# Performance work log

Measured on AMD Instinct MI355X. Metric: run time of the kernel, lower is better.

The kernel has to match this reference:

```python
import jax, jax.numpy as jnp
import numpy as np

B, C, N, K, COUT, W32 = 4, 64, 4096, 16, 64, 32
EPS = 1e-5  # BatchNorm eps


def conv1x1(x, w, b):
    # x: (B, Cin, K, N), w: (Cout, Cin), b: (Cout,)
    return jnp.einsum('oi,bikn->bokn', w, x) + b[None, :, None, None]


def batchnorm(x, gamma, beta):
    # training-mode BN over (B, K, N) per channel
    m = x.mean(axis=(0, 2, 3), keepdims=True)
    v = x.var(axis=(0, 2, 3), keepdims=True)
    return gamma[None, :, None, None] * (x - m) * jax.lax.rsqrt(v + EPS) + beta[None, :, None, None]


def setup_inputs() -> dict:
    key = jax.random.key(0)
    ks = jax.random.split(key, 14)
    s = 0.1
    return {
        'inputs': jax.random.normal(ks[0], (B, C, N), jnp.float32),
        'inputs_pos': jax.random.normal(ks[1], (B, 3, N), jnp.float32),
        'inverse_density': jax.random.uniform(ks[2], (B, 1, N), jnp.float32),
        # WeightNet: Conv2d(3, 32, 1) + BN(32)
        'wn_w': jax.random.normal(ks[3], (W32, 3), jnp.float32) * s,
        'wn_b': jnp.zeros((W32,), jnp.float32),
        'wn_g': jnp.ones((W32,), jnp.float32),
        'wn_be': jnp.zeros((W32,), jnp.float32),
        # DensityNet: Conv2d(1,16,1)+BN(16), Conv2d(16,1,1)
        'dn_w1': jax.random.normal(ks[4], (16, 1), jnp.float32) * s,
        'dn_b1': jnp.zeros((16,), jnp.float32),
        'dn_g1': jnp.ones((16,), jnp.float32),
        'dn_be1': jnp.zeros((16,), jnp.float32),
        'dn_w2': jax.random.normal(ks[5], (1, 16), jnp.float32) * s,
        'dn_b2': jnp.zeros((1,), jnp.float32),
        # Linear(C*32, COUT)
        'lin_w': jax.random.normal(ks[6], (COUT, C * W32), jnp.float32) * (1.0 / np.sqrt(C * W32)),
        'lin_b': jnp.zeros((COUT,), jnp.float32),
    }


def reference(inputs, inputs_pos, inverse_density,
              wn_w, wn_b, wn_g, wn_be,
              dn_w1, dn_b1, dn_g1, dn_be1, dn_w2, dn_b2,
              lin_w, lin_b):
    b, c, n = inputs.shape
    # pairwise squared distances (B, N, N); stride=1 so no FPS sampling
    sq = jnp.sum(inputs_pos ** 2, axis=1)  # (B, N)
    dist = sq[:, :, None] + sq[:, None, :] - 2.0 * jnp.einsum('bdi,bdj->bij', inputs_pos, inputs_pos)
    _, nn_idx = jax.lax.top_k(-dist, K)  # (B, N, K) nearest neighbors (incl. self)

    def gather(x, idx):  # x: (Cx, N), idx: (N, K) -> (Cx, K, N)
        return jnp.transpose(x[:, idx], (0, 2, 1))

    nn_pos = jax.vmap(gather)(inputs_pos, nn_idx)        # (B, 3, K, N)
    nn_inputs = jax.vmap(gather)(inputs, nn_idx)         # (B, C, K, N)
    lnn_pos = nn_pos - inputs_pos[:, :, None, :]         # translated neighbor positions
    nn_inv_d = jax.vmap(gather)(inverse_density, nn_idx)  # (B, 1, K, N)

    density_scale = nn_inv_d / nn_inv_d.max(axis=2, keepdims=True)
    h = jax.nn.relu(batchnorm(conv1x1(density_scale, dn_w1, dn_b1), dn_g1, dn_be1))
    density_scale = jax.nn.sigmoid(conv1x1(h, dn_w2, dn_b2))  # (B, 1, K, N)

    scaled = nn_inputs * density_scale                    # (B, C, K, N)
    weights = jax.nn.relu(batchnorm(conv1x1(lnn_pos, wn_w, wn_b), wn_g, wn_be))  # (B, 32, K, N)

    # per-point matmul: (B,N,C,K) @ (B,N,K,32) -> (B,N,C,32)
    feat = jnp.einsum('bckn,bwkn->bncw', scaled, weights).reshape(b, n, c * W32)
    out = feat @ lin_w.T + lin_b                          # (B, N, COUT)
    return jnp.transpose(out, (0, 2, 1))                  # (B, COUT, N)
```

## Files before the change

kernel.cpp:

```cpp
#include <hip/hip_runtime.h>
#include <math.h>

#define NB 4
#define NC 64
#define NPTS 4096
#define NROWS (NB*NPTS)

typedef __attribute__((ext_vector_type(4))) float f32x4;
typedef __bf16 bf16x8 __attribute__((ext_vector_type(8)));

__device__ __forceinline__ ushort f2bf(float f) {
  unsigned u = __float_as_uint(f);
  u = (u + 0x7FFFu + ((u >> 16) & 1u)) >> 16;
  return (ushort)u;
}
__device__ __forceinline__ unsigned pk2(float lo, float hi) {
  return (unsigned)f2bf(lo) | ((unsigned)f2bf(hi) << 16);
}

__device__ __forceinline__ void insert16(double dist, int j, double (&dd)[16], int (&ii)[16]) {
  double cd = dist; int ci = j;
#pragma unroll
  for (int s = 0; s < 16; ++s) {
    double od = dd[s]; int oi = ii[s];
    bool c = cd < od;
    dd[s] = c ? cd : od;
    ii[s] = c ? ci : oi;
    cd = c ? od : cd;
    ci = c ? oi : ci;
  }
}

__device__ __forceinline__ void bub16u(unsigned key, unsigned (&t)[16]) {
#pragma unroll
  for (int q2 = 0; q2 < 16; ++q2) {
    unsigned lo = min(key, t[q2]);
    key = max(key, t[q2]);
    t[q2] = lo;
  }
}

#define DPPD(RES, V, CTRL) { \
  long long bits_ = __double_as_longlong(V); \
  int lo_ = (int)bits_, hi_ = (int)(bits_ >> 32); \
  int lo2_ = __builtin_amdgcn_update_dpp(0, lo_, CTRL, 0xF, 0xF, true); \
  int hi2_ = __builtin_amdgcn_update_dpp(0, hi_, CTRL, 0xF, 0xF, true); \
  RES = __longlong_as_double(((long long)(unsigned)lo2_) | ((long long)hi2_ << 32)); }

__device__ __forceinline__ double wave_reduce(double v) {
  double t2;
  DPPD(t2, v, 0x121) v += t2;
  DPPD(t2, v, 0x122) v += t2;
  DPPD(t2, v, 0x124) v += t2;
  DPPD(t2, v, 0x128) v += t2;
  v += __shfl_xor(v, 16, 64);
  v += __shfl_xor(v, 32, 64);
  return v;
}

__global__ __launch_bounds__(256) void prep_all(const float* __restrict__ pos,
                                                float4* __restrict__ pos4,
                                                const float* __restrict__ in,
                                                ushort* __restrict__ inT,
                                                const float* __restrict__ lin_w,
                                                ushort* __restrict__ LTf) {
  __shared__ float tile[64][68];
  int t = threadIdx.x;
  int bid = blockIdx.x;
  if (bid < 64) {
    int g = bid * 256 + t;
    int b = g >> 12, n = g & (NPTS - 1);
    const float* pb = pos + b * 3 * NPTS;
    pos4[g] = make_float4(pb[n], pb[NPTS + n], pb[2 * NPTS + n], 0.f);
  } else if (bid < 320) {
    int blk = bid - 64;
    int b = blk >> 6;
    int n0 = (blk & 63) << 6;
    {
      int c = t >> 2, q = t & 3;
      const float* src = in + ((size_t)(b * 64 + c)) * NPTS + n0 + q * 16;
      float4 v0 = ((const float4*)src)[0];
      float4 v1 = ((const float4*)src)[1];
      float4 v2 = ((const float4*)src)[2];
      float4 v3 = ((const float4*)src)[3];
      *(float4*)&tile[c][q * 16 + 0] = v0;
      *(float4*)&tile[c][q * 16 + 4] = v1;
      *(float4*)&tile[c][q * 16 + 8] = v2;
      *(float4*)&tile[c][q * 16 + 12] = v3;
    }
    __syncthreads();
    {
      int nl = t >> 2, cq = t & 3;
      unsigned pk[8];
#pragma unroll
      for (int i = 0; i < 8; ++i) {
        float lo = tile[cq * 16 + 2 * i][nl];
        float hi = tile[cq * 16 + 2 * i + 1][nl];
        pk[i] = pk2(lo, hi);
      }
      uint4* dst = (uint4*)(inT + ((size_t)(b * NPTS + n0 + nl)) * 64 + cq * 16);
      dst[0] = make_uint4(pk[0], pk[1], pk[2], pk[3]);
      dst[1] = make_uint4(pk[4], pk[5], pk[6], pk[7]);
    }
  } else {
    int g = (bid - 320) * 256 + t;
    int l = g & 63, ot = (g >> 6) & 3, s = g >> 8;
    int o = ot * 16 + (l & 15);
    const float* src = lin_w + (size_t)o * 2048 + s * 32 + (l >> 4) * 8;
    float4 u0 = ((const float4*)src)[0];
    float4 u1 = ((const float4*)src)[1];
    ((uint4*)LTf)[g] = make_uint4(pk2(u0.x, u0.y), pk2(u0.z, u0.w),
                                  pk2(u1.x, u1.y), pk2(u1.z, u1.w));
  }
}

__global__ __launch_bounds__(256) void knn_sub(const float4* __restrict__ pos4,
                                               uint4* __restrict__ partials) {
  __shared__ float4 cand[128];
  int t = threadIdx.x;
  int row0 = blockIdx.x * 256;
  int b = row0 >> 12;
  int y = blockIdx.y;
  int j0 = (y >> 1) * 1024 + (y & 1) * 128;
  const float4* pb = pos4 + b * NPTS;
  if (t < 128) cand[t] = pb[j0 + t];
  __syncthreads();
  float4 q = pb[(row0 + t) & (NPTS - 1)];
  unsigned dd[16];
#pragma unroll
  for (int s = 0; s < 16; ++s) dd[s] = 0xFFFFFFFFu;
#pragma unroll 4
  for (int jj = 0; jj < 128; ++jj) {
    float4 c = cand[jj];
    float dx = q.x - c.x, dy = q.y - c.y, dz = q.z - c.z;
    float d = fmaf(dx, dx, fmaf(dy, dy, dz * dz));
    unsigned key = (__float_as_uint(d) & 0xFFFFF000u) | (unsigned)(j0 + jj);
#pragma unroll
    for (int s = 0; s < 16; ++s) {
      unsigned lo = min(key, dd[s]);
      key = max(key, dd[s]);
      dd[s] = lo;
    }
  }
  uint4* po = partials + ((size_t)y * NROWS + row0 + t) * 4;
  po[0] = make_uint4(dd[0], dd[1], dd[2], dd[3]);
  po[1] = make_uint4(dd[4], dd[5], dd[6], dd[7]);
  po[2] = make_uint4(dd[8], dd[9], dd[10], dd[11]);
  po[3] = make_uint4(dd[12], dd[13], dd[14], dd[15]);
}

__global__ __launch_bounds__(64) void knn_thresh(const uint4* __restrict__ partials,
                                                 unsigned* __restrict__ T0g) {
  __shared__ unsigned sl[64 * 132];
  int tid = threadIdx.x;
  int row0 = blockIdx.x * 64;
  uint4* sl4 = (uint4*)sl;
  size_t base = (size_t)row0 * 4 + tid;
#define TW(IT, V) { int g2 = ((IT) & 3) * 64 + tid; \
                    sl4[(g2 >> 2) * 33 + ((IT) >> 2) * 4 + (g2 & 3)] = (V); }
#define TB(B) { int IT0 = (B) * 8; \
  uint4 w0 = partials[(size_t)((IT0+0)>>2)*(NROWS*4) + ((IT0+0)&3)*64 + base]; \
  uint4 w1 = partials[(size_t)((IT0+1)>>2)*(NROWS*4) + ((IT0+1)&3)*64 + base]; \
  uint4 w2 = partials[(size_t)((IT0+2)>>2)*(NROWS*4) + ((IT0+2)&3)*64 + base]; \
  uint4 w3 = partials[(size_t)((IT0+3)>>2)*(NROWS*4) + ((IT0+3)&3)*64 + base]; \
  uint4 w4 = partials[(size_t)((IT0+4)>>2)*(NROWS*4) + ((IT0+4)&3)*64 + base]; \
  uint4 w5 = partials[(size_t)((IT0+5)>>2)*(NROWS*4) + ((IT0+5)&3)*64 + base]; \
  uint4 w6 = partials[(size_t)((IT0+6)>>2)*(NROWS*4) + ((IT0+6)&3)*64 + base]; \
  uint4 w7 = partials[(size_t)((IT0+7)>>2)*(NROWS*4) + ((IT0+7)&3)*64 + base]; \
  TW(IT0+0,w0) TW(IT0+1,w1) TW(IT0+2,w2) TW(IT0+3,w3) \
  TW(IT0+4,w4) TW(IT0+5,w5) TW(IT0+6,w6) TW(IT0+7,w7) }
  TB(0) TB(1) TB(2) TB(3)
#undef TB
#undef TW
  __syncthreads();
  unsigned top[16];
#pragma unroll
  for (int s = 0; s < 16; ++s) top[s] = 0xFFFFFFFFu;
  const unsigned* my = sl + tid * 132;
  for (int y = 0; y < 8; ++y) {
#pragma unroll 4
    for (int s = 0; s < 16; ++s) {
      unsigned key = my[y * 16 + s];
      if (key >= top[15]) break;
#pragma unroll
      for (int q2 = 0; q2 < 16; ++q2) {
        unsigned lo = min(key, top[q2]);
        key = max(key, top[q2]);
        top[q2] = lo;
      }
    }
  }
  T0g[row0 + tid] = top[15] & 0xFFFFF000u;
}

__global__ __launch_bounds__(256) void knn_filter(const float4* __restrict__ pos4,
                                                  const unsigned* __restrict__ T0g,
                                                  uint4* __restrict__ surv) {
  __shared__ float4 cand[256];
  __shared__ unsigned lq[256 * 28];
  int t = threadIdx.x;
  int row0 = blockIdx.x * 256;
  int b = row0 >> 12;
  int y = blockIdx.y;
  int j0 = y * 256;
  const float4* pb = pos4 + b * NPTS;
  cand[t] = pb[j0 + t];
  __syncthreads();
  int r = row0 + t;
  float4 q = pb[r & (NPTS - 1)];
  unsigned T = T0g[r];
  unsigned cnt = 0;
  unsigned* myq = lq + t * 28;
#pragma unroll 4
  for (int jj = 0; jj < 256; ++jj) {
    float4 c = cand[jj];
    float dx = q.x - c.x, dy = q.y - c.y, dz = q.z - c.z;
    float d = fmaf(dx, dx, fmaf(dy, dy, dz * dz));
    unsigned m = __float_as_uint(d) & 0xFFFFF000u;
    if (m <= T) {
      if (cnt < 28u) myq[cnt] = m | (unsigned)(j0 + jj);
      ++cnt;
    }
  }
  cnt = cnt < 28u ? cnt : 28u;
  unsigned t16[16];
#pragma unroll
  for (int s = 0; s < 16; ++s) t16[s] = 0xFFFFFFFFu;
  const uint4* qsrc = (const uint4*)myq;
  uint4 q0 = qsrc[0], q1 = qsrc[1], q2 = qsrc[2], q3 = qsrc[3],
        q4 = qsrc[4], q5 = qsrc[5], q6 = qsrc[6];
#define SIN(K, I) { if ((I) < cnt) bub16u((K), t16); }
  SIN(q0.x,0u) SIN(q0.y,1u) SIN(q0.z,2u) SIN(q0.w,3u)
  SIN(q1.x,4u) SIN(q1.y,5u) SIN(q1.z,6u) SIN(q1.w,7u)
  SIN(q2.x,8u) SIN(q2.y,9u) SIN(q2.z,10u) SIN(q2.w,11u)
  SIN(q3.x,12u) SIN(q3.y,13u) SIN(q3.z,14u) SIN(q3.w,15u)
  SIN(q4.x,16u) SIN(q4.y,17u) SIN(q4.z,18u) SIN(q4.w,19u)
  SIN(q5.x,20u) SIN(q5.y,21u) SIN(q5.z,22u) SIN(q5.w,23u)
  SIN(q6.x,24u) SIN(q6.y,25u) SIN(q6.z,26u) SIN(q6.w,27u)
#undef SIN
  uint4* dst = surv + ((size_t)r * 16 + y) * 4;
  dst[0] = make_uint4(t16[0], t16[1], t16[2], t16[3]);
  dst[1] = make_uint4(t16[4], t16[5], t16[6], t16[7]);
  dst[2] = make_uint4(t16[8], t16[9], t16[10], t16[11]);
  dst[3] = make_uint4(t16[12], t16[13], t16[14], t16[15]);
}

__global__ __launch_bounds__(256) void knn_final(const float4* __restrict__ pos4,
                                                 const float* __restrict__ invd,
                                                 const uint4* __restrict__ surv,
                                                 int* __restrict__ nn_idx,
                                                 float* __restrict__ dsbuf,
                                                 double* __restrict__ stp) {
  int t = threadIdx.x;
  int ln = t & 15;
  int r = blockIdx.x * 16 + (t >> 4);
  int b = r >> 12, n = r & (NPTS - 1);

  const uint4* sp = surv + ((size_t)r * 16 + ln) * 4;
  uint4 u0 = sp[0], u1 = sp[1], u2 = sp[2], u3 = sp[3];
  unsigned h0=u0.x,h1=u0.y,h2=u0.z,h3=u0.w,h4=u1.x,h5=u1.y,h6=u1.z,h7=u1.w,
           h8=u2.x,h9=u2.y,h10=u2.z,h11=u2.w,h12=u3.x,h13=u3.y,h14=u3.z,h15=u3.w;
  unsigned t0,t1,t2,t3,t4,t5,t6,t7,t8,t9,t10,t11,t12,t13,t14,t15,t16;
#define UMIN_DPP(M, CTRL) \
  M = min(M, (unsigned)__builtin_amdgcn_update_dpp(0, (int)(M), CTRL, 0xF, 0xF, true));
#define RND(TT) { unsigned m = h0; \
  UMIN_DPP(m, 0x121) UMIN_DPP(m, 0x122) UMIN_DPP(m, 0x124) UMIN_DPP(m, 0x128) \
  TT = m; bool pop = (h0 == m); \
  h0 = pop ? h1 : h0;  h1 = pop ? h2 : h1;  h2 = pop ? h3 : h2; \
  h3 = pop ? h4 : h3;  h4 = pop ? h5 : h4;  h5 = pop ? h6 : h5; \
  h6 = pop ? h7 : h6;  h7 = pop ? h8 : h7;  h8 = pop ? h9 : h8; \
  h9 = pop ? h10 : h9; h10 = pop ? h11 : h10; h11 = pop ? h12 : h11; \
  h12 = pop ? h13 : h12; h13 = pop ? h14 : h13; h14 = pop ? h15 : h14; \
  h15 = pop ? 0xFFFFFFFFu : h15; }
  RND(t0) RND(t1) RND(t2) RND(t3) RND(t4) RND(t5) RND(t6) RND(t7)
  RND(t8) RND(t9) RND(t10) RND(t11) RND(t12) RND(t13) RND(t14) RND(t15)
  RND(t16)

  const float4* pb = pos4 + b * NPTS;
  float4 qp = pb[n];
  double xi = qp.x, yi = qp.y, zi = qp.z;

  int jm;
  bool tie = ((t15 & 0xFFFFF000u) == (t16 & 0xFFFFF000u));
  if (!tie) {
    unsigned tm = t0;
    tm = (ln == 1) ? t1 : tm;   tm = (ln == 2) ? t2 : tm;
    tm = (ln == 3) ? t3 : tm;   tm = (ln == 4) ? t4 : tm;
    tm = (ln == 5) ? t5 : tm;   tm = (ln == 6) ? t6 : tm;
    tm = (ln == 7) ? t7 : tm;   tm = (ln == 8) ? t8 : tm;
    tm = (ln == 9) ? t9 : tm;   tm = (ln == 10) ? t10 : tm;
    tm = (ln == 11) ? t11 : tm; tm = (ln == 12) ? t12 : tm;
    tm = (ln == 13) ? t13 : tm; tm = (ln == 14) ? t14 : tm;
    tm = (ln == 15) ? t15 : tm;
    jm = (int)(tm & 0xFFFu);
  } else {
    unsigned t17, t18, t19, t20, t21, t22, t23;
    RND(t17) RND(t18) RND(t19) RND(t20) RND(t21) RND(t22) RND(t23)
    double dd[16]; int ii[16];
#pragma unroll
    for (int s = 0; s < 16; ++s) { dd[s] = 1e300; ii[s] = 0; }
#define RRK(TT) if (TT != 0xFFFFFFFFu) { int j = (int)(TT & 0xFFFu); \
  float4 cj = pb[j]; \
  double dx = xi - (double)cj.x, dy = yi - (double)cj.y, dz = zi - (double)cj.z; \
  double dist = dx * dx + dy * dy + dz * dz; \
  if (dist < dd[15]) insert16(dist, j, dd, ii); }
    RRK(t0) RRK(t1) RRK(t2) RRK(t3) RRK(t4) RRK(t5) RRK(t6) RRK(t7)
    RRK(t8) RRK(t9) RRK(t10) RRK(t11) RRK(t12) RRK(t13) RRK(t14) RRK(t15)
    RRK(t16) RRK(t17) RRK(t18) RRK(t19) RRK(t20) RRK(t21) RRK(t22) RRK(t23)
#undef RRK
    int jj2 = ii[0];
#pragma unroll
    for (int s = 1; s < 16; ++s) jj2 = (ln == s) ? ii[s] : jj2;
    jm = jj2;
  }
#undef RND
#undef UMIN_DPP

  nn_idx[(size_t)r * 16 + ln] = jm;
  const float* ivb = invd + b * NPTS;
  float v = ivb[jm];
  float vmax = v;
#define FMAX_DPP(X, CTRL) { \
    float y_ = __int_as_float(__builtin_amdgcn_update_dpp(0, __float_as_int(X), CTRL, 0xF, 0xF, true)); \
    X = fmaxf(X, y_); }
  FMAX_DPP(vmax, 0x121) FMAX_DPP(vmax, 0x122)
  FMAX_DPP(vmax, 0x124) FMAX_DPP(vmax, 0x128)
#undef FMAX_DPP
  float x = v / vmax;
  dsbuf[(size_t)r * 16 + ln] = x;

  double sx = x, sxx = (double)x * (double)x;
  float4 pj = pb[jm];
  double lx = (double)pj.x - xi, lyv = (double)pj.y - yi, lzv = (double)pj.z - zi;
  double l1x = lx, l1y = lyv, l1z = lzv;
  double lxx = lx * lx, lyy = lyv * lyv, lzz = lzv * lzv;
  double lxy = lx * lyv, lxz = lx * lzv, lyz = lyv * lzv;
  sx  = wave_reduce(sx);  sxx = wave_reduce(sxx);
  l1x = wave_reduce(l1x); l1y = wave_reduce(l1y); l1z = wave_reduce(l1z);
  lxx = wave_reduce(lxx); lyy = wave_reduce(lyy); lzz = wave_reduce(lzz);
  lxy = wave_reduce(lxy); lxz = wave_reduce(lxz); lyz = wave_reduce(lyz);
  if ((t & 63) == 0) {
    double* o = stp + ((size_t)blockIdx.x * 4 + (t >> 6)) * 16;
    o[0] = sx;  o[1] = sxx;
    o[2] = l1x; o[3] = l1y; o[4] = l1z;
    o[5] = lxx; o[6] = lyy; o[7] = lzz;
    o[8] = lxy; o[9] = lxz; o[10] = lyz;
  }
}

__global__ __launch_bounds__(256) void finalize_params(const double* __restrict__ stp,
                                const float* __restrict__ wn_w,
                                const float* __restrict__ wn_g,
                                const float* __restrict__ wn_be,
                                const float* __restrict__ dn_w1,
                                const float* __restrict__ dn_g1,
                                const float* __restrict__ dn_be1,
                                float* __restrict__ prm) {
  __shared__ double part[16][16];
  __shared__ double red[11];
  const double M = (double)NROWS * 16.0;
  int t = threadIdx.x;
  {
    int c = t & 15, ch = t >> 4;
    double s = 0.0;
#pragma unroll 8
    for (int w = 0; w < 256; ++w) s += stp[(size_t)(ch * 256 + w) * 16 + c];
    part[ch][c] = s;
  }
  __syncthreads();
  if (t < 11) {
    double s = 0.0;
#pragma unroll
    for (int ch = 0; ch < 16; ++ch) s += part[ch][t];
    red[t] = s;
  }
  __syncthreads();
  if (t < 32) {
    double m0 = red[2] / M, m1 = red[3] / M, m2 = red[4] / M;
    double cxx = red[5] / M - m0 * m0, cyy = red[6] / M - m1 * m1, czz = red[7] / M - m2 * m2;
    double cxy = red[8] / M - m0 * m1, cxz = red[9] / M - m0 * m2, cyz = red[10] / M - m1 * m2;
    double w0 = wn_w[t * 3], w1 = wn_w[t * 3 + 1], w2 = wn_w[t * 3 + 2];
    double var = w0 * w0 * cxx + w1 * w1 * cyy + w2 * w2 * czz
               + 2.0 * (w0 * w1 * cxy + w0 * w2 * cxz + w1 * w2 * cyz);
    double alpha = (double)wn_g[t] / sqrt(var + 1e-5);
    double a0 = alpha * w0, a1 = alpha * w1, a2 = alpha * w2;
    prm[t * 3] = (float)a0; prm[t * 3 + 1] = (float)a1; prm[t * 3 + 2] = (float)a2;
    prm[96 + t] = (float)((double)wn_be[t] - (a0 * m0 + a1 * m1 + a2 * m2));
  } else if (t < 48) {
    int ch = t - 32;
    double mx = red[0] / M;
    double vx = red[1] / M - mx * mx;
    double w = dn_w1[ch];
    double alpha = (double)dn_g1[ch] * w / sqrt(w * w * vx + 1e-5);
    prm[128 + ch] = (float)alpha;
    prm[144 + ch] = (float)((double)dn_be1[ch] - alpha * mx);
  }
}

#define XSTR 2320
#define WTOFF 37120
#define WTSTR 1040

__global__ __launch_bounds__(256, 3) void fused(const ushort* __restrict__ inT,
                                                const float4* __restrict__ pos4,
                                                const int* __restrict__ nn_idx,
                                                const float* __restrict__ dsbuf,
                                                const float* __restrict__ prm_g,
                                                const float* __restrict__ dn_w2,
                                                const float* __restrict__ dn_b2,
                                                const ushort* __restrict__ LTf,
                                                const float* __restrict__ lin_b,
                                                float* __restrict__ out) {
  __shared__ __align__(16) char smem[53760];
  char* xraw = smem;
  char* wT = smem + WTOFF;
  int t = threadIdx.x;
  int blk = blockIdx.x;
  int b = blk >> 8;
  int n0 = (blk & 255) << 4;
  {
    int k = t >> 4, p = t & 15;
    int r = blk * 16 + p;
    int n = n0 + p;
    int j = nn_idx[(size_t)r * 16 + k];
    float4 pj = pos4[b * NPTS + j];
    float4 pn = pos4[b * NPTS + n];
    float lx = pj.x - pn.x, ly = pj.y - pn.y, lz = pj.z - pn.z;
    float xr = dsbuf[(size_t)r * 16 + k];
    float sacc = dn_b2[0];
#pragma unroll
    for (int ch = 0; ch < 16; ++ch)
      sacc = fmaf(dn_w2[ch], fmaxf(fmaf(prm_g[128 + ch], xr, prm_g[144 + ch]), 0.f), sacc);
    float ds = 1.f / (1.f + expf(-sacc));
    const uint4* srcx = (const uint4*)(inT + ((size_t)(b * NPTS + j)) * 64);
    uint4* dstx = (uint4*)(xraw + p * XSTR + k * 144);
#pragma unroll
    for (int i = 0; i < 8; ++i) dstx[i] = srcx[i];
    char* wr = wT + p * WTSTR + k * 2;
#pragma unroll
    for (int w = 0; w < 32; ++w) {
      float v = fmaf(prm_g[w * 3], lx,
                fmaf(prm_g[w * 3 + 1], ly,
                fmaf(prm_g[w * 3 + 2], lz, prm_g[96 + w])));
      *(ushort*)(wr + w * 32) = f2bf(fmaxf(v, 0.f) * ds);
    }
  }
  __syncthreads();
  int wv = t >> 6;
  int l = t & 63;
  int lr = l & 15;
  int q = l >> 4;
  int kq8 = (q & 1) * 1152;
  int swz = (lr & 7) << 4;
  const f32x4 zf = (f32x4)0.f;
  uint4 zu = make_uint4(0u, 0u, 0u, 0u);

#define DECLD(IT) unsigned d##IT##_0,d##IT##_1,d##IT##_2,d##IT##_3,d##IT##_4, \
  d##IT##_5,d##IT##_6,d##IT##_7,d##IT##_8,d##IT##_9,d##IT##_10,d##IT##_11, \
  d##IT##_12,d##IT##_13,d##IT##_14,d##IT##_15;
  DECLD(0) DECLD(1) DECLD(2) DECLD(3)
#undef DECLD

#define LOADB(BU, NI, XP) { \
    const char* xb = (XP) + ((NI) * 16 + lr) * 2; \
    unsigned e0 = *(const ushort*)(xb); \
    unsigned e1 = *(const ushort*)(xb + 144); \
    unsigned e2 = *(const ushort*)(xb + 288); \
    unsigned e3 = *(const ushort*)(xb + 432); \
    unsigned e4 = *(const ushort*)(xb + 576); \
    unsigned e5 = *(const ushort*)(xb + 720); \
    unsigned e6 = *(const ushort*)(xb + 864); \
    unsigned e7 = *(const ushort*)(xb + 1008); \
    BU = make_uint4(e0 | (e1 << 16), e2 | (e3 << 16), \
                    e4 | (e5 << 16), e6 | (e7 << 16)); }

#define MM(AF, BF, RA, RB) { \
    f32x4 D = __builtin_amdgcn_mfma_f32_16x16x32_bf16(AF, BF, zf, 0, 0, 0); \
    RA = pk2(D.x, D.y); RB = pk2(D.z, D.w); }

#define DO_POINT(IT) { \
    int p = wv * 4 + (IT); \
    const char* wtp = wT + p * WTSTR; \
    const char* xp = xraw + p * XSTR + kq8; \
    uint4 a0u = zu, a1u = zu; \
    if (q < 2) { \
      a0u = *(const uint4*)(wtp + lr * 32 + q * 16); \
      a1u = *(const uint4*)(wtp + (16 + lr) * 32 + q * 16); \
    } \
    bf16x8 A0 = *reinterpret_cast<bf16x8*>(&a0u); \
    bf16x8 A1 = *reinterpret_cast<bf16x8*>(&a1u); \
    uint4 b0u, b1u, b2u, b3u; \
    LOADB(b0u, 0, xp) LOADB(b1u, 1, xp) LOADB(b2u, 2, xp) LOADB(b3u, 3, xp) \
    bf16x8 B0 = *reinterpret_cast<bf16x8*>(&b0u); \
    bf16x8 B1 = *reinterpret_cast<bf16x8*>(&b1u); \
    bf16x8 B2 = *reinterpret_cast<bf16x8*>(&b2u); \
    bf16x8 B3 = *reinterpret_cast<bf16x8*>(&b3u); \
    MM(A0, B0, d##IT##_0, d##IT##_1)   MM(A0, B1, d##IT##_2, d##IT##_3) \
    MM(A0, B2, d##IT##_4, d##IT##_5)   MM(A0, B3, d##IT##_6, d##IT##_7) \
    MM(A1, B0, d##IT##_8, d##IT##_9)   MM(A1, B1, d##IT##_10, d##IT##_11) \
    MM(A1, B2, d##IT##_12, d##IT##_13) MM(A1, B3, d##IT##_14, d##IT##_15) }

  DO_POINT(0) DO_POINT(1) DO_POINT(2) DO_POINT(3)
#undef DO_POINT
#undef MM
#undef LOADB
  __syncthreads();
  int hq = q >> 1;
  int m0 = (q & 1) * 2;
  const uint4* Lq = (const uint4*)LTf;
  f32x4 cacc = (f32x4)0.f;
#define STT(IT, MI, NIL, RA, RB) { \
    int p = wv * 4 + (IT); \
    int h = (MI) * 2 + hq; \
    int base = (((NIL) * 16 + lr)) * 1024 + (p + 16 * h) * 16 + m0 * 4; \
    *(unsigned*)(smem + (base ^ swz)) = RA; \
    *(unsigned*)(smem + ((base + 4) ^ swz)) = RB; }
#define STPA(IT) \
    STT(IT,0,0,d##IT##_0,d##IT##_1)   STT(IT,0,1,d##IT##_2,d##IT##_3) \
    STT(IT,1,0,d##IT##_8,d##IT##_9)   STT(IT,1,1,d##IT##_10,d##IT##_11)
  STPA(0) STPA(1) STPA(2) STPA(3)
#undef STPA
  __syncthreads();
#pragma unroll 4
  for (int s = 0; s < 32; ++s) {
    uint4 ua = *(const uint4*)(smem + (((s * 64 + l) * 16) ^ ((s & 7) << 4)));
    uint4 ub = Lq[(s * 4 + wv) * 64 + l];
    bf16x8 A = *reinterpret_cast<bf16x8*>(&ua);
    bf16x8 B = *reinterpret_cast<bf16x8*>(&ub);
    cacc = __builtin_amdgcn_mfma_f32_16x16x32_bf16(A, B, cacc, 0, 0, 0);
  }
  __syncthreads();
#define STPB(IT) \
    STT(IT,0,0,d##IT##_4,d##IT##_5)   STT(IT,0,1,d##IT##_6,d##IT##_7) \
    STT(IT,1,0,d##IT##_12,d##IT##_13) STT(IT,1,1,d##IT##_14,d##IT##_15)
  STPB(0) STPB(1) STPB(2) STPB(3)
#undef STPB
#undef STT
  __syncthreads();
#pragma unroll 4
  for (int sl2 = 0; sl2 < 32; ++sl2) {
    int s = sl2 + 32;
    uint4 ua = *(const uint4*)(smem + (((sl2 * 64 + l) * 16) ^ ((sl2 & 7) << 4)));
    uint4 ub = Lq[(s * 4 + wv) * 64 + l];
    bf16x8 A = *reinterpret_cast<bf16x8*>(&ua);
    bf16x8 B = *reinterpret_cast<bf16x8*>(&ub);
    cacc = __builtin_amdgcn_mfma_f32_16x16x32_bf16(A, B, cacc, 0, 0, 0);
  }
  {
    int o = wv * 16 + lr;
    float bias = lin_b[o];
    cacc.x += bias; cacc.y += bias; cacc.z += bias; cacc.w += bias;
    *(f32x4*)(out + ((size_t)(b * 64 + o)) * NPTS + n0 + q * 4) = cacc;
  }
}

extern "C" void kernel_launch(void* const* d_in, const int* in_sizes, int n_in,
                              void* d_out, int out_size, void* d_ws, size_t ws_size,
                              hipStream_t stream) {
  (void)in_sizes; (void)n_in; (void)out_size; (void)ws_size;
  const float* inputs = (const float*)d_in[0];
  const float* pos    = (const float*)d_in[1];
  const float* invd   = (const float*)d_in[2];
  const float* wn_w   = (const float*)d_in[3];
  const float* wn_g   = (const float*)d_in[5];
  const float* wn_be  = (const float*)d_in[6];
  const float* dn_w1  = (const float*)d_in[7];
  const float* dn_g1  = (const float*)d_in[9];
  const float* dn_be1 = (const float*)d_in[10];
  const float* dn_w2  = (const float*)d_in[11];
  const float* dn_b2  = (const float*)d_in[12];
  const float* lin_w  = (const float*)d_in[13];
  const float* lin_b  = (const float*)d_in[14];
  float* outp = (float*)d_out;

  char* ws = (char*)d_ws;
  float*    prm      = (float*)(ws + 1024);
  float4*   pos4     = (float4*)(ws + 4096);
  int*      nnidx    = (int*)(ws + (size_t)(1u << 19));
  float*    dsbuf    = (float*)(ws + (size_t)(3u << 19));
  ushort*   inT      = (ushort*)(ws + (size_t)(5u << 19));
  ushort*   LTf      = (ushort*)(ws + (size_t)(9u << 19));
  unsigned* T0g      = (unsigned*)(ws + (size_t)(19u << 18));
  double*   stp      = (double*)(ws + (size_t)(5u << 20));
  uint4*    partials = (uint4*)(ws + (size_t)(11u << 19));
  uint4*    surv     = (uint4*)(ws + (size_t)(11u << 19));

  prep_all<<<384, 256, 0, stream>>>(pos, pos4, inputs, inT, lin_w, LTf);
  knn_sub<<<dim3(64, 8), 256, 0, stream>>>(pos4, partials);
  knn_thresh<<<256, 64, 0, stream>>>(partials, T0g);
  knn_filter<<<dim3(64, 16), 256, 0, stream>>>(pos4, T0g, surv);
  knn_final<<<1024, 256, 0, stream>>>(pos4, invd, surv, nnidx, dsbuf, stp);
  finalize_params<<<1, 256, 0, stream>>>(stp, wn_w, wn_g, wn_be, dn_w1, dn_g1, dn_be1, prm);
  fused<<<1024, 256, 0, stream>>>(inT, pos4, nnidx, dsbuf, prm, dn_w2, dn_b2, LTf, lin_b, outp);
}
```

Measured before the change: 136.4 us.

## Fuse KNN filter and final merge into one kernel, dropping survivor buffer

Merges the threshold-filter pass and the cross-segment merge into a single kernel. Each 16-lane group now handles one query row, and each lane scans one 256-candidate segment. All 4096 batch positions are staged into LDS as padded SoA arrays, so the per-segment top-16 lists stay in registers and feed the DPP merge directly. This removes the global survivor buffer write/read and one launch. In exchange each block redundantly loads the whole batch's positions and uses about 77 KB of LDS, which limits occupancy.

```diff
diff --git a/kernel.cpp b/kernel.cpp
--- a/kernel.cpp
+++ b/kernel.cpp
@@ -193,28 +193,39 @@
   T0g[row0 + tid] = top[15] & 0xFFFFF000u;
 }
 
-__global__ __launch_bounds__(256) void knn_filter(const float4* __restrict__ pos4,
-                                                  const unsigned* __restrict__ T0g,
-                                                  uint4* __restrict__ surv) {
-  __shared__ float4 cand[256];
+__global__ __launch_bounds__(256, 2) void knn_ff(const float4* __restrict__ pos4,
+                                                 const float* __restrict__ invd,
+                                                 const unsigned* __restrict__ T0g,
+                                                 int* __restrict__ nn_idx,
+                                                 float* __restrict__ dsbuf,
+                                                 double* __restrict__ stp) {
+  __shared__ float cx[16 * 258], cy[16 * 258], cz[16 * 258];
   __shared__ unsigned lq[256 * 28];
   int t = threadIdx.x;
-  int row0 = blockIdx.x * 256;
-  int b = row0 >> 12;
-  int y = blockIdx.y;
-  int j0 = y * 256;
+  int blk = blockIdx.x;
+  int r = blk * 16 + (t >> 4);
+  int b = r >> 12, n = r & (NPTS - 1);
+  int ln = t & 15;
   const float4* pb = pos4 + b * NPTS;
-  cand[t] = pb[j0 + t];
-  __syncthreads();
-  int r = row0 + t;
-  float4 q = pb[r & (NPTS - 1)];
+#pragma unroll
+  for (int i = 0; i < 16; ++i) {
+    int g = i * 256 + t;
+    float4 c = pb[g];
+    int off = (g >> 8) * 258 + (g & 255);
+    cx[off] = c.x; cy[off] = c.y; cz[off] = c.z;
+  }
+  __syncthreads();
+  float4 q = pb[n];
   unsigned T = T0g[r];
   unsigned cnt = 0;
   unsigned* myq = lq + t * 28;
+  int j0 = ln * 256;
+  const float* cxp = cx + ln * 258;
+  const float* cyp = cy + ln * 258;
+  const float* czp = cz + ln * 258;
 #pragma unroll 4
   for (int jj = 0; jj < 256; ++jj) {
-    float4 c = cand[jj];
-    float dx = q.x - c.x, dy = q.y - c.y, dz = q.z - c.z;
+    float dx = q.x - cxp[jj], dy = q.y - cyp[jj], dz = q.z - czp[jj];
     float d = fmaf(dx, dx, fmaf(dy, dy, dz * dz));
     unsigned m = __float_as_uint(d) & 0xFFFFF000u;
     if (m <= T) {
@@ -223,13 +234,13 @@
     }
   }
   cnt = cnt < 28u ? cnt : 28u;
-  unsigned t16[16];
-#pragma unroll
-  for (int s = 0; s < 16; ++s) t16[s] = 0xFFFFFFFFu;
+  unsigned t16a[16];
+#pragma unroll
+  for (int s = 0; s < 16; ++s) t16a[s] = 0xFFFFFFFFu;
   const uint4* qsrc = (const uint4*)myq;
   uint4 q0 = qsrc[0], q1 = qsrc[1], q2 = qsrc[2], q3 = qsrc[3],
         q4 = qsrc[4], q5 = qsrc[5], q6 = qsrc[6];
-#define SIN(K, I) { if ((I) < cnt) bub16u((K), t16); }
+#define SIN(K, I) { if ((I) < cnt) bub16u((K), t16a); }
   SIN(q0.x,0u) SIN(q0.y,1u) SIN(q0.z,2u) SIN(q0.w,3u)
   SIN(q1.x,4u) SIN(q1.y,5u) SIN(q1.z,6u) SIN(q1.w,7u)
   SIN(q2.x,8u) SIN(q2.y,9u) SIN(q2.z,10u) SIN(q2.w,11u)
@@ -238,28 +249,9 @@
   SIN(q5.x,20u) SIN(q5.y,21u) SIN(q5.z,22u) SIN(q5.w,23u)
   SIN(q6.x,24u) SIN(q6.y,25u) SIN(q6.z,26u) SIN(q6.w,27u)
 #undef SIN
-  uint4* dst = surv + ((size_t)r * 16 + y) * 4;
-  dst[0] = make_uint4(t16[0], t16[1], t16[2], t16[3]);
-  dst[1] = make_uint4(t16[4], t16[5], t16[6], t16[7]);
-  dst[2] = make_uint4(t16[8], t16[9], t16[10], t16[11]);
-  dst[3] = make_uint4(t16[12], t16[13], t16[14], t16[15]);
-}
-
-__global__ __launch_bounds__(256) void knn_final(const float4* __restrict__ pos4,
-                                                 const float* __restrict__ invd,
-                                                 const uint4* __restrict__ surv,
-                                                 int* __restrict__ nn_idx,
-                                                 float* __restrict__ dsbuf,
-                                                 double* __restrict__ stp) {
-  int t = threadIdx.x;
-  int ln = t & 15;
-  int r = blockIdx.x * 16 + (t >> 4);
-  int b = r >> 12, n = r & (NPTS - 1);
-
-  const uint4* sp = surv + ((size_t)r * 16 + ln) * 4;
-  uint4 u0 = sp[0], u1 = sp[1], u2 = sp[2], u3 = sp[3];
-  unsigned h0=u0.x,h1=u0.y,h2=u0.z,h3=u0.w,h4=u1.x,h5=u1.y,h6=u1.z,h7=u1.w,
-           h8=u2.x,h9=u2.y,h10=u2.z,h11=u2.w,h12=u3.x,h13=u3.y,h14=u3.z,h15=u3.w;
+  unsigned h0=t16a[0],h1=t16a[1],h2=t16a[2],h3=t16a[3],h4=t16a[4],h5=t16a[5],
+           h6=t16a[6],h7=t16a[7],h8=t16a[8],h9=t16a[9],h10=t16a[10],h11=t16a[11],
+           h12=t16a[12],h13=t16a[13],h14=t16a[14],h15=t16a[15];
   unsigned t0,t1,t2,t3,t4,t5,t6,t7,t8,t9,t10,t11,t12,t13,t14,t15,t16;
 #define UMIN_DPP(M, CTRL) \
   M = min(M, (unsigned)__builtin_amdgcn_update_dpp(0, (int)(M), CTRL, 0xF, 0xF, true));
@@ -276,8 +268,7 @@
   RND(t8) RND(t9) RND(t10) RND(t11) RND(t12) RND(t13) RND(t14) RND(t15)
   RND(t16)
 
-  const float4* pb = pos4 + b * NPTS;
-  float4 qp = pb[n];
+  float4 qp = q;
   double xi = qp.x, yi = qp.y, zi = qp.z;
 
   int jm;
@@ -340,7 +331,7 @@
   lxx = wave_reduce(lxx); lyy = wave_reduce(lyy); lzz = wave_reduce(lzz);
   lxy = wave_reduce(lxy); lxz = wave_reduce(lxz); lyz = wave_reduce(lyz);
   if ((t & 63) == 0) {
-    double* o = stp + ((size_t)blockIdx.x * 4 + (t >> 6)) * 16;
+    double* o = stp + ((size_t)blk * 4 + (t >> 6)) * 16;
     o[0] = sx;  o[1] = sxx;
     o[2] = l1x; o[3] = l1y; o[4] = l1z;
     o[5] = lxx; o[6] = lyy; o[7] = lzz;
@@ -583,13 +574,11 @@
   unsigned* T0g      = (unsigned*)(ws + (size_t)(19u << 18));
   double*   stp      = (double*)(ws + (size_t)(5u << 20));
   uint4*    partials = (uint4*)(ws + (size_t)(11u << 19));
-  uint4*    surv     = (uint4*)(ws + (size_t)(11u << 19));
 
   prep_all<<<384, 256, 0, stream>>>(pos, pos4, inputs, inT, lin_w, LTf);
   knn_sub<<<dim3(64, 8), 256, 0, stream>>>(pos4, partials);
   knn_thresh<<<256, 64, 0, stream>>>(partials, T0g);
-  knn_filter<<<dim3(64, 16), 256, 0, stream>>>(pos4, T0g, surv);
-  knn_final<<<1024, 256, 0, stream>>>(pos4, invd, surv, nnidx, dsbuf, stp);
+  knn_ff<<<1024, 256, 0, stream>>>(pos4, invd, T0g, nnidx, dsbuf, stp);
   finalize_params<<<1, 256, 0, stream>>>(stp, wn_w, wn_g, wn_be, dn_w1, dn_g1, dn_be1, prm);
   fused<<<1024, 256, 0, stream>>>(inT, pos4, nnidx, dsbuf, prm, dn_w2, dn_b2, LTf, lin_b, outp);
 }
```

New measurement: 154.8 us. 13.5% more time.
